# Optimization experiments

Measured on AMD Instinct MI355X. Metric: run time of the kernel, lower is better.

Reference implementation:

```python
import jax, jax.numpy as jnp
import numpy as np

B_SZ, SEQ, H = 8, 1024, 2048
LN_EPS = 1e-6
CLIP = 1.0e6


def setup_inputs() -> dict:
    key = jax.random.key(0)
    ks = jax.random.split(key, 8)
    lecun = 1.0 / np.sqrt(H)
    return {
        "x": jax.random.normal(ks[0], (B_SZ, SEQ, H), dtype=jnp.float32),
        "context": jnp.zeros((B_SZ, H), dtype=jnp.float32),
        # learned params
        "A": -jax.random.uniform(ks[1], (H,), dtype=jnp.float32),  # diagonal decay (zeros-init in src; small negative for stable decay)
        "Bm": jax.random.normal(ks[2], (H, H), dtype=jnp.float32) * lecun,
        "Cm": jax.random.normal(ks[3], (H, H), dtype=jnp.float32) * lecun,
        "dt_kernel": jax.random.normal(ks[4], (H, 1), dtype=jnp.float32) * 0.02,
        "dt_bias": jnp.zeros((1,), dtype=jnp.float32),
        "gate_kernel": jax.random.normal(ks[5], (H, H), dtype=jnp.float32) * lecun,
        "gate_bias": jnp.zeros((H,), dtype=jnp.float32),
        "ln_scale": jnp.ones((H,), dtype=jnp.float32),
        "ln_bias": jnp.zeros((H,), dtype=jnp.float32),
    }


def _layernorm(x, scale, bias):
    mu = jnp.mean(x, axis=-1, keepdims=True)
    var = jnp.mean(jnp.square(x - mu), axis=-1, keepdims=True)
    return (x - mu) * jax.lax.rsqrt(var + LN_EPS) * scale + bias


def reference(x, context, A, Bm, Cm, dt_kernel, dt_bias, gate_kernel, gate_bias, ln_scale, ln_bias):
    xn = jnp.clip(_layernorm(x, ln_scale, ln_bias), -CLIP, CLIP)  # [B,S,H]
    xt = jnp.swapaxes(xn, 0, 1)  # time-major [S,B,H]

    def step(state, x_t):
        # x_t: [B,H]; delta: [B,1] from Dense(1)
        delta = jnp.exp(x_t @ dt_kernel + dt_bias)
        decay = jnp.exp(delta * A)                  # [B,H] via broadcast
        new_state = state * decay + x_t @ Bm        # [B,H]
        out = new_state @ Cm                        # [B,H]
        return new_state, out

    final_state, ys = jax.lax.scan(step, context, xt)
    outputs = jnp.swapaxes(ys, 0, 1)  # [B,S,H]
    gate = outputs @ gate_kernel + gate_bias
    outputs = outputs * jax.nn.sigmoid(gate)  # GLU
    # dropout deterministic (training=False) -> identity
    return outputs, final_state
```

## Files before the change

### kernel.cpp

```cpp
#include <hip/hip_runtime.h>
#include <hip/hip_bf16.h>

#define H_DIM 2048
#define B_SZ  8
#define SEQ   1024
#define M_DIM (B_SZ*SEQ)
#define KDIM  2048
#define NKT   (KDIM/64)
#define CCH   32
#define CLEN  (SEQ/CCH)

using f32x4 = __attribute__((ext_vector_type(4))) float;
using s16x8 = __attribute__((ext_vector_type(8))) short;

__device__ __forceinline__ float bf2f(unsigned short u) {
  unsigned int x = ((unsigned int)u) << 16;
  return __builtin_bit_cast(float, x);
}
__device__ __forceinline__ unsigned short f2bf(float f) {
  unsigned int x = __builtin_bit_cast(unsigned int, f);
  unsigned int r = (x + 0x7fffu + ((x >> 16) & 1u)) >> 16;
  return (unsigned short)r;
}

__device__ __forceinline__ void gl_lds16(const void* g, void* l) {
  __builtin_amdgcn_global_load_lds(
      (__attribute__((address_space(1))) void*)g,
      (__attribute__((address_space(3))) void*)l, 16, 0, 0);
}

__global__ __launch_bounds__(256) void transpose_kernel(
    const float* __restrict__ src, unsigned short* __restrict__ dst, int R, int C)
{
  __shared__ float t[32][33];
  int tx = threadIdx.x & 31, ty = threadIdx.x >> 5;
  int c0 = blockIdx.x << 5, r0 = blockIdx.y << 5;
#pragma unroll
  for (int i = 0; i < 32; i += 8)
    t[ty + i][tx] = src[(size_t)(r0 + ty + i) * C + (c0 + tx)];
  __syncthreads();
#pragma unroll
  for (int i = 0; i < 32; i += 8)
    dst[(size_t)(c0 + ty + i) * R + (r0 + tx)] = f2bf(t[tx][ty + i]);
}

__global__ __launch_bounds__(256) void ln_delta_kernel(
    const float* __restrict__ x, const float* __restrict__ lns,
    const float* __restrict__ lnb, const float* __restrict__ dtk,
    const float* __restrict__ dtb, unsigned short* __restrict__ xn,
    float* __restrict__ delta)
{
  const int row = blockIdx.x;
  const int tid = threadIdx.x;
  const float* xr = x + (size_t)row * H_DIM;
  float v[8];
  *(float4*)&v[0] = ((const float4*)xr)[tid * 2];
  *(float4*)&v[4] = ((const float4*)xr)[tid * 2 + 1];
  float s1 = 0.f, s2 = 0.f;
#pragma unroll
  for (int j = 0; j < 8; ++j) { s1 += v[j]; s2 += v[j] * v[j]; }
  __shared__ float red[8];
#pragma unroll
  for (int off = 32; off; off >>= 1) {
    s1 += __shfl_down(s1, off);
    s2 += __shfl_down(s2, off);
  }
  if ((tid & 63) == 0) { red[tid >> 6] = s1; red[4 + (tid >> 6)] = s2; }
  __syncthreads();
  float mean = (red[0] + red[1] + red[2] + red[3]) * (1.0f / H_DIM);
  float var  = (red[4] + red[5] + red[6] + red[7]) * (1.0f / H_DIM) - mean * mean;
  float rstd = rsqrtf(var + 1e-6f);

  float sc[8], bi[8], dk[8];
  *(float4*)&sc[0] = ((const float4*)lns)[tid * 2];
  *(float4*)&sc[4] = ((const float4*)lns)[tid * 2 + 1];
  *(float4*)&bi[0] = ((const float4*)lnb)[tid * 2];
  *(float4*)&bi[4] = ((const float4*)lnb)[tid * 2 + 1];
  *(float4*)&dk[0] = ((const float4*)dtk)[tid * 2];
  *(float4*)&dk[4] = ((const float4*)dtk)[tid * 2 + 1];

  float dot = 0.f;
  s16x8 o;
#pragma unroll
  for (int j = 0; j < 8; ++j) {
    float xv = (v[j] - mean) * rstd * sc[j] + bi[j];
    xv = fminf(fmaxf(xv, -1.0e6f), 1.0e6f);
    dot += xv * dk[j];
    o[j] = (short)f2bf(xv);
  }
  *(s16x8*)(xn + (size_t)row * H_DIM + tid * 8) = o;

  __syncthreads();
#pragma unroll
  for (int off = 32; off; off >>= 1) dot += __shfl_down(dot, off);
  if ((tid & 63) == 0) red[tid >> 6] = dot;
  __syncthreads();
  if (tid == 0)
    delta[row] = __expf(red[0] + red[1] + red[2] + red[3] + dtb[0]);
}

__global__ __launch_bounds__(256) void scan1_kernel(
    const unsigned short* __restrict__ U, const float* __restrict__ delta,
    const float* __restrict__ Adiag, float* __restrict__ Q, float* __restrict__ P)
{
  const int h = blockIdx.x * 1024 + threadIdx.x * 4;
  const int c = blockIdx.y, b = blockIdx.z;
  const float4 a = *(const float4*)(Adiag + h);
  const unsigned short* u = U + ((size_t)b * SEQ + c * CLEN) * H_DIM + h;
  const float* dl = delta + b * SEQ + c * CLEN;
  float4 st = {0.f, 0.f, 0.f, 0.f};
  float4 pr = {1.f, 1.f, 1.f, 1.f};
#pragma unroll 8
  for (int s = 0; s < CLEN; ++s) {
    const float d = dl[s];
    const ushort4 uv = *(const ushort4*)(u + (size_t)s * H_DIM);
    const float dx = __expf(d * a.x), dy = __expf(d * a.y);
    const float dz = __expf(d * a.z), dw = __expf(d * a.w);
    st.x = fmaf(st.x, dx, bf2f(uv.x)); st.y = fmaf(st.y, dy, bf2f(uv.y));
    st.z = fmaf(st.z, dz, bf2f(uv.z)); st.w = fmaf(st.w, dw, bf2f(uv.w));
    pr.x *= dx; pr.y *= dy; pr.z *= dz; pr.w *= dw;
  }
  const size_t idx = ((size_t)b * CCH + c) * H_DIM + h;
  *(float4*)(Q + idx) = st;
  *(float4*)(P + idx) = pr;
}

__global__ __launch_bounds__(256) void scan2_kernel(
    const float* __restrict__ Q, const float* __restrict__ P,
    const float* __restrict__ ctx, float* __restrict__ sIn,
    float* __restrict__ finalSt)
{
  const int h = blockIdx.x * 256 + threadIdx.x;
  const int b = blockIdx.y;
  float s = ctx[b * H_DIM + h];
#pragma unroll
  for (int c = 0; c < CCH; ++c) {
    const size_t idx = ((size_t)b * CCH + c) * H_DIM + h;
    sIn[idx] = s;
    s = fmaf(s, P[idx], Q[idx]);
  }
  finalSt[b * H_DIM + h] = s;
}

__global__ __launch_bounds__(256) void scan3_kernel(
    const unsigned short* __restrict__ U, const float* __restrict__ delta,
    const float* __restrict__ Adiag, const float* __restrict__ sIn,
    unsigned short* __restrict__ states)
{
  const int h = blockIdx.x * 1024 + threadIdx.x * 4;
  const int c = blockIdx.y, b = blockIdx.z;
  const float4 a = *(const float4*)(Adiag + h);
  const unsigned short* u = U + ((size_t)b * SEQ + c * CLEN) * H_DIM + h;
  unsigned short* so = states + ((size_t)b * SEQ + c * CLEN) * H_DIM + h;
  const float* dl = delta + b * SEQ + c * CLEN;
  float4 st = *(const float4*)(sIn + ((size_t)b * CCH + c) * H_DIM + h);
#pragma unroll 8
  for (int s = 0; s < CLEN; ++s) {
    const float d = dl[s];
    const ushort4 uv = *(const ushort4*)(u + (size_t)s * H_DIM);
    const float dx = __expf(d * a.x), dy = __expf(d * a.y);
    const float dz = __expf(d * a.z), dw = __expf(d * a.w);
    st.x = fmaf(st.x, dx, bf2f(uv.x)); st.y = fmaf(st.y, dy, bf2f(uv.y));
    st.z = fmaf(st.z, dz, bf2f(uv.z)); st.w = fmaf(st.w, dw, bf2f(uv.w));
    ushort4 ov = { f2bf(st.x), f2bf(st.y), f2bf(st.z), f2bf(st.w) };
    *(ushort4*)(so + (size_t)s * H_DIM) = ov;
  }
}


#define BAR_() { __builtin_amdgcn_sched_barrier(0); __builtin_amdgcn_s_barrier(); __builtin_amdgcn_sched_barrier(0); }
#define VMC(N) asm volatile("s_waitcnt vmcnt(" #N ")" ::: "memory");

#define RD_A03(PA0, PA1) { _Pragma("unroll") for (int i_ = 0; i_ < 4; ++i_) { \
    a0[i_] = *(const s16x8*)((PA0) + i_ * 4096); \
    a1[i_] = *(const s16x8*)((PA1) + i_ * 4096); } }
#define RD_A47(PA0, PA1) { _Pragma("unroll") for (int i_ = 0; i_ < 4; ++i_) { \
    a0[i_] = *(const s16x8*)((PA0) + 16384 + i_ * 4096); \
    a1[i_] = *(const s16x8*)((PA1) + 16384 + i_ * 4096); } }
#define RD_B01(PB0, PB1) { _Pragma("unroll") for (int j_ = 0; j_ < 2; ++j_) { \
    bq0[j_] = *(const s16x8*)((PB0) + j_ * 8192); \
    bq1[j_] = *(const s16x8*)((PB1) + j_ * 8192); } }
#define RD_B23(PB0, PB1) { _Pragma("unroll") for (int j_ = 2; j_ < 4; ++j_) { \
    bq0[j_] = *(const s16x8*)((PB0) + j_ * 8192); \
    bq1[j_] = *(const s16x8*)((PB1) + j_ * 8192); } }

#define Q_MM(IB, JB) { __builtin_amdgcn_s_setprio(1); \
  _Pragma("unroll") for (int i_ = 0; i_ < 4; ++i_) \
  _Pragma("unroll") for (int j_ = 0; j_ < 2; ++j_) { \
    acc[(IB)+i_][(JB)+j_] = __builtin_amdgcn_mfma_f32_16x16x32_bf16(a0[i_], bq0[(JB)+j_], acc[(IB)+i_][(JB)+j_], 0, 0, 0); \
    acc[(IB)+i_][(JB)+j_] = __builtin_amdgcn_mfma_f32_16x16x32_bf16(a1[i_], bq1[(JB)+j_], acc[(IB)+i_][(JB)+j_], 0, 0, 0); } \
  __builtin_amdgcn_s_setprio(0); }

#define STAGE_A(BUF, HH, TT) { const char* s_ = srcA + (HH) * 524288 + (TT) * 128; \
  char* d_ = ldsA + (BUF) * 32768 + (HH) * 16384 + tid16; \
  gl_lds16(s_, d_); gl_lds16(s_ + 262144, d_ + 8192); }
#define STAGE_B(BUF, HH, TT) { const char* s_ = srcB + (HH) * 524288 + (TT) * 128; \
  char* d_ = ldsB + (BUF) * 32768 + (HH) * 16384 + tid16; \
  gl_lds16(s_, d_); gl_lds16(s_ + 8192, d_ + 8192); }

#undef STAGE_B
#define STAGE_B(BUF, HH, TT) { const char* s_ = srcB + (HH) * 524288 + (TT) * 128; \
  char* d_ = ldsB + (BUF) * 32768 + (HH) * 16384 + tid16; \
  gl_lds16(s_, d_); gl_lds16(s_ + 262144, d_ + 8192); }

template <int EPI>
__global__ __launch_bounds__(512, 2) void gemm8p(
    const char* __restrict__ Ab, const char* __restrict__ Bb,
    float* __restrict__ outF, unsigned short* __restrict__ outH,
    const unsigned short* __restrict__ Ybf, const float* __restrict__ gbias)
{
  extern __shared__ char lds[];
  char* ldsA = lds;
  char* ldsB = lds + 65536;

  const int tid  = threadIdx.x;
  const int lane = tid & 63, wid = tid >> 6;
  const int wr = wid >> 2, wc = wid & 3;
  const int fr = lane & 15, kq = lane >> 4;

  const int bid  = blockIdx.x;
  const int wgid = (bid & 7) * 32 + (bid >> 3);
  const int bm = wgid & 31, bn = wgid >> 5;

  const int grow = tid >> 3;
  const int gswz = ((tid & 7) ^ (grow & 7)) << 4;
  const char* srcA = Ab + ((size_t)(bm * 256 + grow)) * 4096 + gswz;
  const char* srcB = Bb + ((size_t)(bn * 256 + grow)) * 4096 + gswz;
  const int tid16 = tid << 4;

  const int sw0 = ((kq ^ (fr & 7)) << 4);
  const int sw1 = (((4 | kq) ^ (fr & 7)) << 4);
  const char* pa0b0 = ldsA + wr * 2048 + fr * 128 + sw0;
  const char* pa1b0 = ldsA + wr * 2048 + fr * 128 + sw1;
  const char* pa0b1 = pa0b0 + 32768;
  const char* pa1b1 = pa1b0 + 32768;
  const char* pb0b0 = ldsB + wc * 2048 + fr * 128 + sw0;
  const char* pb1b0 = ldsB + wc * 2048 + fr * 128 + sw1;
  const char* pb0b1 = pb0b0 + 32768;
  const char* pb1b1 = pb1b0 + 32768;

  f32x4 acc[8][4] = {};
  s16x8 a0[4], a1[4], bq0[4], bq1[4];

  STAGE_A(0, 0, 0); STAGE_B(0, 0, 0); STAGE_B(0, 1, 0); STAGE_A(0, 1, 0);
  STAGE_A(1, 0, 1); STAGE_B(1, 0, 1); STAGE_B(1, 1, 1);
  VMC(6);
  BAR_();

  for (int t = 0; t < NKT / 2 - 1; ++t) {
    const int T0 = 2 * t;
    RD_A03(pa0b0, pa1b0); RD_B01(pb0b0, pb1b0);
    STAGE_A(1, 1, T0 + 1);
    BAR_(); Q_MM(0, 0); BAR_();
    RD_B23(pb0b0, pb1b0);
    STAGE_A(0, 0, T0 + 2);
    BAR_(); Q_MM(0, 2); BAR_();
    RD_A47(pa0b0, pa1b0);
    STAGE_B(0, 0, T0 + 2);
    BAR_(); Q_MM(4, 0); BAR_();
    STAGE_B(0, 1, T0 + 2);
    BAR_(); Q_MM(4, 2); VMC(6); BAR_();
    RD_A03(pa0b1, pa1b1); RD_B01(pb0b1, pb1b1);
    STAGE_A(0, 1, T0 + 2);
    BAR_(); Q_MM(0, 0); BAR_();
    RD_B23(pb0b1, pb1b1);
    STAGE_A(1, 0, T0 + 3);
    BAR_(); Q_MM(0, 2); BAR_();
    RD_A47(pa0b1, pa1b1);
    STAGE_B(1, 0, T0 + 3);
    BAR_(); Q_MM(4, 0); BAR_();
    STAGE_B(1, 1, T0 + 3);
    BAR_(); Q_MM(4, 2); VMC(6); BAR_();
  }

  RD_A03(pa0b0, pa1b0); RD_B01(pb0b0, pb1b0);
  STAGE_A(1, 1, 31);
  BAR_(); Q_MM(0, 0); BAR_();
  RD_B23(pb0b0, pb1b0);
  BAR_(); Q_MM(0, 2); BAR_();
  RD_A47(pa0b0, pa1b0);
  BAR_(); Q_MM(4, 0); BAR_();
  BAR_(); Q_MM(4, 2); VMC(0); BAR_();
  RD_A03(pa0b1, pa1b1); RD_B01(pb0b1, pb1b1);
  BAR_(); Q_MM(0, 0); BAR_();
  RD_B23(pb0b1, pb1b1);
  BAR_(); Q_MM(0, 2); BAR_();
  RD_A47(pa0b1, pa1b1);
  BAR_(); Q_MM(4, 0); BAR_();
  Q_MM(4, 2);

  const int cr = (lane >> 4) << 2;
  const int cc = lane & 15;
#pragma unroll
  for (int i = 0; i < 8; ++i) {
#pragma unroll
    for (int j = 0; j < 4; ++j) {
#pragma unroll
      for (int r = 0; r < 4; ++r) {
        const size_t row = (size_t)bm * 256 + (2 * i + wr) * 16 + cr + r;
        const size_t col = (size_t)bn * 256 + (4 * j + wc) * 16 + cc;
        const float v = acc[i][j][r];
        if constexpr (EPI == 1) {
          outH[row * H_DIM + col] = f2bf(v);
        } else {
          const float g = v + gbias[col];
          const float y = bf2f(Ybf[row * H_DIM + col]);
          outF[row * H_DIM + col] = y * (1.0f / (1.0f + __expf(-g)));
        }
      }
    }
  }
}

extern "C" void kernel_launch(void* const* d_in, const int* in_sizes, int n_in,
                              void* d_out, int out_size, void* d_ws, size_t ws_size,
                              hipStream_t stream) {
  (void)in_sizes; (void)n_in; (void)out_size; (void)ws_size;
  const float* x     = (const float*)d_in[0];
  const float* ctx   = (const float*)d_in[1];
  const float* Adiag = (const float*)d_in[2];
  const float* Bm    = (const float*)d_in[3];
  const float* Cm    = (const float*)d_in[4];
  const float* dtk   = (const float*)d_in[5];
  const float* dtb   = (const float*)d_in[6];
  const float* gk    = (const float*)d_in[7];
  const float* gb    = (const float*)d_in[8];
  const float* lns   = (const float*)d_in[9];
  const float* lnb   = (const float*)d_in[10];
  float* outF = (float*)d_out;

  char* ws = (char*)d_ws;
  unsigned short* xnY    = (unsigned short*)ws; ws += (size_t)M_DIM * H_DIM * 2;
  unsigned short* U      = (unsigned short*)ws; ws += (size_t)M_DIM * H_DIM * 2;
  unsigned short* states = (unsigned short*)ws; ws += (size_t)M_DIM * H_DIM * 2;
  unsigned short* T1     = (unsigned short*)ws; ws += (size_t)H_DIM * H_DIM * 2;
  unsigned short* T2     = (unsigned short*)ws; ws += (size_t)H_DIM * H_DIM * 2;
  unsigned short* T3     = (unsigned short*)ws; ws += (size_t)H_DIM * H_DIM * 2;
  float* delta           = (float*)ws;          ws += (size_t)M_DIM * 4;
  float* Qbuf            = (float*)ws;          ws += (size_t)B_SZ * CCH * H_DIM * 4;
  float* Pbuf            = (float*)ws;          ws += (size_t)B_SZ * CCH * H_DIM * 4;
  float* sInBuf          = (float*)ws;          ws += (size_t)B_SZ * CCH * H_DIM * 4;

  hipFuncSetAttribute((const void*)&gemm8p<1>,
                      hipFuncAttributeMaxDynamicSharedMemorySize, 131072);
  hipFuncSetAttribute((const void*)&gemm8p<2>,
                      hipFuncAttributeMaxDynamicSharedMemorySize, 131072);

  dim3 tb(256);
  transpose_kernel<<<dim3(64, 64), tb, 0, stream>>>(Bm, T1, H_DIM, H_DIM);
  transpose_kernel<<<dim3(64, 64), tb, 0, stream>>>(Cm, T2, H_DIM, H_DIM);
  transpose_kernel<<<dim3(64, 64), tb, 0, stream>>>(gk, T3, H_DIM, H_DIM);
  ln_delta_kernel<<<M_DIM, tb, 0, stream>>>(x, lns, lnb, dtk, dtb, xnY, delta);
  gemm8p<1><<<256, 512, 131072, stream>>>(
      (const char*)xnY, (const char*)T1, nullptr, U, nullptr, nullptr);
  scan1_kernel<<<dim3(H_DIM / 1024, CCH, B_SZ), tb, 0, stream>>>(
      U, delta, Adiag, Qbuf, Pbuf);
  scan2_kernel<<<dim3(H_DIM / 256, B_SZ), tb, 0, stream>>>(
      Qbuf, Pbuf, ctx, sInBuf, outF + (size_t)M_DIM * H_DIM);
  scan3_kernel<<<dim3(H_DIM / 1024, CCH, B_SZ), tb, 0, stream>>>(
      U, delta, Adiag, sInBuf, states);
  gemm8p<1><<<256, 512, 131072, stream>>>(
      (const char*)states, (const char*)T2, nullptr, xnY, nullptr, nullptr);
  gemm8p<2><<<256, 512, 131072, stream>>>(
      (const char*)xnY, (const char*)T3, outF, nullptr, xnY, gb);
}
```

Measured before the change: 257.9 us.

## Stage GEMM epilogue through LDS for coalesced stores and remap tile-to-XCD assignment

The GEMM epilogue now writes accumulators into swizzled LDS and then issues 16-byte coalesced global stores, instead of scattered 2- or 4-byte per-element stores. The GLU path also does vectorized loads of bias and Y. The block-to-tile mapping is changed so each XCD handles a compact 8x4 region of output tiles, which is meant to improve L2 reuse of A and B. A duplicate STAGE_B macro definition is removed. The cost is extra LDS round-trips and barriers in the epilogue.

New measurement: 256.6 us. Within noise of the previous version (-0.5%).

```diff
diff --git a/kernel.cpp b/kernel.cpp
--- a/kernel.cpp
+++ b/kernel.cpp
@@ -196,11 +196,6 @@
   gl_lds16(s_, d_); gl_lds16(s_ + 262144, d_ + 8192); }
 #define STAGE_B(BUF, HH, TT) { const char* s_ = srcB + (HH) * 524288 + (TT) * 128; \
   char* d_ = ldsB + (BUF) * 32768 + (HH) * 16384 + tid16; \
-  gl_lds16(s_, d_); gl_lds16(s_ + 8192, d_ + 8192); }
-
-#undef STAGE_B
-#define STAGE_B(BUF, HH, TT) { const char* s_ = srcB + (HH) * 524288 + (TT) * 128; \
-  char* d_ = ldsB + (BUF) * 32768 + (HH) * 16384 + tid16; \
   gl_lds16(s_, d_); gl_lds16(s_ + 262144, d_ + 8192); }
 
 template <int EPI>
@@ -218,9 +213,11 @@
   const int wr = wid >> 2, wc = wid & 3;
   const int fr = lane & 15, kq = lane >> 4;
 
-  const int bid  = blockIdx.x;
-  const int wgid = (bid & 7) * 32 + (bid >> 3);
-  const int bm = wgid & 31, bn = wgid >> 5;
+  const int bid = blockIdx.x;
+  const int xcd = bid & 7;
+  const int li  = bid >> 3;
+  const int bm  = (xcd >> 1) * 8 + (li & 7);
+  const int bn  = (xcd & 1) * 4 + (li >> 3);
 
   const int grow = tid >> 3;
   const int gswz = ((tid & 7) ^ (grow & 7)) << 4;
@@ -289,24 +286,60 @@
   BAR_(); Q_MM(4, 0); BAR_();
   Q_MM(4, 2);
 
+  __syncthreads();
   const int cr = (lane >> 4) << 2;
   const int cc = lane & 15;
-#pragma unroll
-  for (int i = 0; i < 8; ++i) {
-#pragma unroll
-    for (int j = 0; j < 4; ++j) {
-#pragma unroll
-      for (int r = 0; r < 4; ++r) {
-        const size_t row = (size_t)bm * 256 + (2 * i + wr) * 16 + cr + r;
-        const size_t col = (size_t)bn * 256 + (4 * j + wc) * 16 + cc;
-        const float v = acc[i][j][r];
-        if constexpr (EPI == 1) {
-          outH[row * H_DIM + col] = f2bf(v);
-        } else {
-          const float g = v + gbias[col];
-          const float y = bf2f(Ybf[row * H_DIM + col]);
-          outF[row * H_DIM + col] = y * (1.0f / (1.0f + __expf(-g)));
+  if constexpr (EPI == 1) {
+#pragma unroll
+    for (int i = 0; i < 8; ++i)
+#pragma unroll
+      for (int j = 0; j < 4; ++j)
+#pragma unroll
+        for (int r = 0; r < 4; ++r) {
+          const int row = (2 * i + wr) * 16 + cr + r;
+          const int col = (4 * j + wc) * 16 + cc;
+          const int off = (row * 512 + col * 2) ^ ((row & 7) << 4);
+          *(unsigned short*)(lds + off) = f2bf(acc[i][j][r]);
         }
+    __syncthreads();
+#pragma unroll
+    for (int it = 0; it < 16; ++it) {
+      const int L = it * 8192 + tid * 16;
+      const int row = L >> 9, inrow = L & 511;
+      const s16x8 v = *(const s16x8*)(lds + (L ^ ((row & 7) << 4)));
+      *(s16x8*)(outH + ((size_t)(bm * 256 + row)) * H_DIM + bn * 256 + (inrow >> 1)) = v;
+    }
+  } else {
+#pragma unroll
+    for (int p = 0; p < 2; ++p) {
+      if (p) __syncthreads();
+#pragma unroll
+      for (int i = 4 * p; i < 4 * p + 4; ++i)
+#pragma unroll
+        for (int j = 0; j < 4; ++j)
+#pragma unroll
+          for (int r = 0; r < 4; ++r) {
+            const int lrow = (2 * i + wr) * 16 + cr + r - 128 * p;
+            const int col = (4 * j + wc) * 16 + cc;
+            const int off = (lrow * 1024 + col * 4) ^ ((lrow & 7) << 4);
+            *(float*)(lds + off) = acc[i][j][r];
+          }
+      __syncthreads();
+#pragma unroll
+      for (int it = 0; it < 16; ++it) {
+        const int L = it * 8192 + tid * 16;
+        const int lrow = L >> 10, inrow = L & 1023;
+        const f32x4 v = *(const f32x4*)(lds + (L ^ ((lrow & 7) << 4)));
+        const size_t growg = (size_t)(bm * 256 + 128 * p + lrow);
+        const int gcol = bn * 256 + (inrow >> 2);
+        const float4 gb4 = *(const float4*)(gbias + gcol);
+        const ushort4 y4 = *(const ushort4*)(Ybf + growg * H_DIM + gcol);
+        float4 o;
+        o.x = bf2f(y4.x) / (1.f + __expf(-(v[0] + gb4.x)));
+        o.y = bf2f(y4.y) / (1.f + __expf(-(v[1] + gb4.y)));
+        o.z = bf2f(y4.z) / (1.f + __expf(-(v[2] + gb4.z)));
+        o.w = bf2f(y4.w) / (1.f + __expf(-(v[3] + gb4.w)));
+        *(float4*)(outF + growg * H_DIM + gcol) = o;
       }
     }
   }
```
